# Performance work log

Hardware: AMD Instinct MI355X
Metric: run time of the kernel (lower is better)

The kernel has to match this reference:

```python
import math
import jax, jax.numpy as jnp
import numpy as np

B, N, D = 256, 64, 64
H, HEAD = D // 4, 4
UNTANH = 0.6
SHARPNESS = 1.0
BSCALE = math.sqrt(2 + math.sqrt(2))
INPUT_DIM = 100
SINK_ITERS = 10
EPS = 1e-8


def buntanh(x, a, s):
    # blended (bounded + un-)tanh: tanh(x) + a*x, variance-rescaled
    return (jnp.tanh(x) + a * x) / s


def rms_norm(x, axes):
    return x * jax.lax.rsqrt(jnp.mean(x * x, axis=axes, keepdims=True) + 1e-6)


def sinkhorn_knopp(x, iters=SINK_ITERS):
    # stable exp then alternating row/col normalization -> ~doubly stochastic
    p = jnp.exp(x - jnp.max(x, axis=(-1, -2), keepdims=True))
    def body(p, _):
        p = p / (jnp.sum(p, axis=-1, keepdims=True) + EPS)
        p = p / (jnp.sum(p, axis=-2, keepdims=True) + EPS)
        return p, None
    p, _ = jax.lax.scan(body, p, None, length=iters)
    return p


def setup_inputs() -> dict:
    key = jax.random.key(0)
    k1, k2, k3, k4, k5 = jax.random.split(key, 5)
    env_input = jax.random.normal(k1, (B, INPUT_DIM), dtype=jnp.float32)
    state = 1e-5 * jax.random.normal(k2, (B, N, D), dtype=jnp.float32)
    scale = 1.0 / math.sqrt(D)
    w1 = jax.random.normal(k3, (B, N, D, D), dtype=jnp.float32) * scale
    w2 = jax.random.normal(k4, (B, N, D, D), dtype=jnp.float32) * scale
    w3 = jax.random.normal(k5, (B, N, D, D), dtype=jnp.float32) * scale
    return {"env_input": env_input, "state": state, "w1": w1, "w2": w2, "w3": w3}


def reference(env_input, state, w1, w2, w3):
    step_state = state  # buffer clone
    prediction = buntanh(jnp.einsum('bnj,bnjk->bnk', step_state, w1), UNTANH, BSCALE)
    keys = buntanh(jnp.einsum('bnj,bnjk->bnk', step_state, w2), UNTANH, BSCALE)
    queries = buntanh(jnp.einsum('bnj,bnjk->bnk', step_state, w3), UNTANH, BSCALE)

    # torch.no_grad() block -> stop_gradient over the whole routing/target calc
    Q = queries.reshape(B, N, H, HEAD).transpose(0, 2, 1, 3)  # [B,H,N,hd]
    K = keys.reshape(B, N, H, HEAD).transpose(0, 2, 1, 3)
    V = prediction.reshape(B, N, H, HEAD).transpose(0, 2, 1, 3)
    raw_A = jnp.einsum('bhnd,bhmd->bhnm', Q, K) / math.sqrt(HEAD)
    raw_A = rms_norm(raw_A, axes=(-1, -2)) * SHARPNESS
    probs = sinkhorn_knopp(raw_A)
    A = jnp.where(probs > 1.0 / N, probs, 0.0)  # sinkhot forward (k-hot)
    routed_V = jnp.einsum('bhnm,bhmd->bhnd', A, V)
    target = routed_V.transpose(0, 2, 1, 3).reshape(B, N, D)

    num_input_nodes = math.ceil(INPUT_DIM / D)
    pad_len = num_input_nodes * D - INPUT_DIM
    env_pad = jnp.pad(env_input, ((0, 0), (0, pad_len))).reshape(B, num_input_nodes, D)
    target = target.at[:, :num_input_nodes, :].set(env_pad)
    target = jax.lax.stop_gradient(target)

    loss_w1 = jnp.mean((prediction - target) ** 2)
    loss_w2 = jnp.mean((keys - step_state) ** 2)
    loss_w3 = jnp.mean((queries - target) ** 2)
    return loss_w1 + loss_w2 + loss_w3
```

## Files before the change

### kernel.cpp

```cpp
#include <hip/hip_runtime.h>
#include <math.h>

#define TOT (256*64*64)
#define EPS_SINK 1e-8f
#define THR (1.0f/64.0f)
#define INV_BSCALE 0.5412658773652741f
#define UNTANH_A 0.6f

typedef float nativef4 __attribute__((ext_vector_type(4)));

static __device__ __forceinline__ float buntanh(float x) {
    return (tanhf(x) + UNTANH_A * x) * INV_BSCALE;
}

#if __has_builtin(__builtin_amdgcn_rcpf)
static __device__ __forceinline__ float fastrcp(float x) {
    return __builtin_amdgcn_rcpf(x);
}
#else
static __device__ __forceinline__ float fastrcp(float x) { return 1.0f / x; }
#endif

__global__ __launch_bounds__(512, 4) void fused_brain_kernel(
    const float* __restrict__ env, const float* __restrict__ state,
    const float* __restrict__ w1, const float* __restrict__ w2,
    const float* __restrict__ w3, float* __restrict__ part)
{
    __shared__ float Ss[64][65];
    __shared__ float Vh[64][33];
    __shared__ float Kh[64][33];
    __shared__ float Qh[64][33];
    __shared__ float redL[8][3];

    const int b    = blockIdx.x >> 1;
    const int half = blockIdx.x & 1;
    const int wave = threadIdx.x >> 6;
    const int l    = threadIdx.x & 63;
    const int r8   = l >> 3;
    const int c8   = l & 7;

    {
        const float* sb = state + (size_t)b * 4096 + threadIdx.x * 8;
        const float4 v0 = *(const float4*)(sb);
        const float4 v1 = *(const float4*)(sb + 4);
        const int row = threadIdx.x >> 3;
        const int col = (threadIdx.x & 7) * 8;
        Ss[row][col + 0] = v0.x; Ss[row][col + 1] = v0.y;
        Ss[row][col + 2] = v0.z; Ss[row][col + 3] = v0.w;
        Ss[row][col + 4] = v1.x; Ss[row][col + 5] = v1.y;
        Ss[row][col + 6] = v1.z; Ss[row][col + 7] = v1.w;
    }
    __syncthreads();

    for (int tt = 0; tt < 24; ++tt) {
        const int task = wave * 24 + tt;
        const int widx = task >> 6;
        const int n    = task & 63;
        const float* __restrict__ w =
            (widx == 0) ? w1 : (widx == 1) ? w2 : w3;
        const float* wp = w + ((size_t)(b * 64 + n)) * 4096 + half * 32 + 4 * c8;

        float a0 = 0.f, a1 = 0.f, a2 = 0.f, a3 = 0.f;
#pragma unroll
        for (int j0 = 0; j0 < 64; j0 += 8) {
            const nativef4 wv =
                __builtin_nontemporal_load((const nativef4*)(wp + (j0 + r8) * 64));
            const float sj = Ss[n][j0 + r8];
            a0 = fmaf(sj, wv.x, a0);
            a1 = fmaf(sj, wv.y, a1);
            a2 = fmaf(sj, wv.z, a2);
            a3 = fmaf(sj, wv.w, a3);
        }
        a0 += __shfl_xor(a0, 8, 64); a0 += __shfl_xor(a0, 16, 64); a0 += __shfl_xor(a0, 32, 64);
        a1 += __shfl_xor(a1, 8, 64); a1 += __shfl_xor(a1, 16, 64); a1 += __shfl_xor(a1, 32, 64);
        a2 += __shfl_xor(a2, 8, 64); a2 += __shfl_xor(a2, 16, 64); a2 += __shfl_xor(a2, 32, 64);
        a3 += __shfl_xor(a3, 8, 64); a3 += __shfl_xor(a3, 16, 64); a3 += __shfl_xor(a3, 32, 64);
        a0 = buntanh(a0); a1 = buntanh(a1); a2 = buntanh(a2); a3 = buntanh(a3);
        if (r8 == 0) {
            float* dst = (widx == 0) ? &Vh[n][4 * c8]
                       : (widx == 1) ? &Kh[n][4 * c8] : &Qh[n][4 * c8];
            dst[0] = a0; dst[1] = a1; dst[2] = a2; dst[3] = a3;
        }
    }
    __syncthreads();

    const int cb = 4 * wave;
    const int rg = r8, cg = c8;

    float p[8][8];
    float ss = 0.f, mx = -1e30f;
    {
        float kq[8][4];
#pragma unroll
        for (int j = 0; j < 8; ++j)
#pragma unroll
            for (int d = 0; d < 4; ++d)
                kq[j][d] = Kh[8 * cg + j][cb + d];
#pragma unroll
        for (int i = 0; i < 8; ++i) {
            const float q0 = Qh[8 * rg + i][cb + 0];
            const float q1 = Qh[8 * rg + i][cb + 1];
            const float q2 = Qh[8 * rg + i][cb + 2];
            const float q3 = Qh[8 * rg + i][cb + 3];
#pragma unroll
            for (int j = 0; j < 8; ++j) {
                const float e = (q0 * kq[j][0] + q1 * kq[j][1] +
                                 q2 * kq[j][2] + q3 * kq[j][3]) * 0.5f;
                p[i][j] = e;
                ss += e * e;
                mx = fmaxf(mx, e);
            }
        }
    }
#pragma unroll
    for (int o = 1; o <= 32; o <<= 1) {
        ss += __shfl_xor(ss, o, 64);
        mx = fmaxf(mx, __shfl_xor(mx, o, 64));
    }
    const float scale = rsqrtf(ss * (1.0f / 4096.0f) + 1e-6f);

#pragma unroll
    for (int i = 0; i < 8; ++i)
#pragma unroll
        for (int j = 0; j < 8; ++j)
            p[i][j] = __expf(scale * (p[i][j] - mx));

    for (int it = 0; it < 10; ++it) {
#pragma unroll
        for (int i = 0; i < 8; ++i) {
            float r = ((p[i][0] + p[i][1]) + (p[i][2] + p[i][3])) +
                      ((p[i][4] + p[i][5]) + (p[i][6] + p[i][7]));
            r += __shfl_xor(r, 1, 64);
            r += __shfl_xor(r, 2, 64);
            r += __shfl_xor(r, 4, 64);
            const float inv = fastrcp(r + EPS_SINK);
#pragma unroll
            for (int j = 0; j < 8; ++j) p[i][j] *= inv;
        }
#pragma unroll
        for (int j = 0; j < 8; ++j) {
            float c = ((p[0][j] + p[1][j]) + (p[2][j] + p[3][j])) +
                      ((p[4][j] + p[5][j]) + (p[6][j] + p[7][j]));
            c += __shfl_xor(c, 8, 64);
            c += __shfl_xor(c, 16, 64);
            c += __shfl_xor(c, 32, 64);
            const float inv = fastrcp(c + EPS_SINK);
#pragma unroll
            for (int i = 0; i < 8; ++i) p[i][j] *= inv;
        }
    }

#pragma unroll
    for (int i = 0; i < 8; ++i)
#pragma unroll
        for (int j = 0; j < 8; ++j)
            p[i][j] = (p[i][j] > THR) ? p[i][j] : 0.f;

    float o8[8][4];
#pragma unroll
    for (int i = 0; i < 8; ++i)
#pragma unroll
        for (int d = 0; d < 4; ++d) o8[i][d] = 0.f;
#pragma unroll
    for (int jh = 0; jh < 8; jh += 4) {
        float vf[4][4];
#pragma unroll
        for (int j = 0; j < 4; ++j)
#pragma unroll
            for (int d = 0; d < 4; ++d)
                vf[j][d] = Vh[8 * cg + jh + j][cb + d];
#pragma unroll
        for (int i = 0; i < 8; ++i)
#pragma unroll
            for (int j = 0; j < 4; ++j) {
                o8[i][0] = fmaf(p[i][jh + j], vf[j][0], o8[i][0]);
                o8[i][1] = fmaf(p[i][jh + j], vf[j][1], o8[i][1]);
                o8[i][2] = fmaf(p[i][jh + j], vf[j][2], o8[i][2]);
                o8[i][3] = fmaf(p[i][jh + j], vf[j][3], o8[i][3]);
            }
    }
#pragma unroll
    for (int i = 0; i < 8; ++i)
#pragma unroll
        for (int d = 0; d < 4; ++d) {
            float v = o8[i][d];
            v += __shfl_xor(v, 1, 64);
            v += __shfl_xor(v, 2, 64);
            v += __shfl_xor(v, 4, 64);
            o8[i][d] = v;
        }

    float tva0 = o8[0][0], tva1 = o8[0][1], tva2 = o8[0][2], tva3 = o8[0][3];
#pragma unroll
    for (int i = 1; i < 8; ++i) {
        if (cg == i) {
            tva0 = o8[i][0]; tva1 = o8[i][1];
            tva2 = o8[i][2]; tva3 = o8[i][3];
        }
    }

    float l1 = 0.f, l2 = 0.f, l3 = 0.f;
    {
        const int n = 8 * rg + cg;
#pragma unroll
        for (int d = 0; d < 4; ++d) {
            const int cl = cb + d;
            const int c  = half * 32 + cl;
            float tv;
            if (n < 2) {
                const int idx = n * 64 + c;
                tv = (idx < 100) ? env[b * 100 + idx] : 0.f;
            } else {
                tv = (d == 0) ? tva0 : (d == 1) ? tva1 : (d == 2) ? tva2 : tva3;
            }
            const float pv = Vh[n][cl];
            const float kk = Kh[n][cl];
            const float qv = Qh[n][cl];
            const float sv = Ss[n][c];
            const float d1 = pv - tv;
            const float d2 = kk - sv;
            const float d3 = qv - tv;
            l1 = fmaf(d1, d1, l1);
            l2 = fmaf(d2, d2, l2);
            l3 = fmaf(d3, d3, l3);
        }
    }
#pragma unroll
    for (int o = 1; o <= 32; o <<= 1) {
        l1 += __shfl_xor(l1, o, 64);
        l2 += __shfl_xor(l2, o, 64);
        l3 += __shfl_xor(l3, o, 64);
    }
    if (l == 0) { redL[wave][0] = l1; redL[wave][1] = l2; redL[wave][2] = l3; }
    __syncthreads();
    if (threadIdx.x == 0) {
        float s1 = 0.f, s2 = 0.f, s3 = 0.f;
#pragma unroll
        for (int wv = 0; wv < 8; ++wv) {
            s1 += redL[wv][0]; s2 += redL[wv][1]; s3 += redL[wv][2];
        }
        part[blockIdx.x]        = s1;
        part[512 + blockIdx.x]  = s2;
        part[1024 + blockIdx.x] = s3;
    }
}

__global__ __launch_bounds__(256) void loss_final_kernel(
    const float* __restrict__ part, float* __restrict__ out)
{
    float a = 0.f;
    for (int i = threadIdx.x; i < 1536; i += 256) a += part[i];
#pragma unroll
    for (int o = 32; o >= 1; o >>= 1) a += __shfl_xor(a, o, 64);
    __shared__ float red[4];
    const int wv = threadIdx.x >> 6, ln = threadIdx.x & 63;
    if (ln == 0) red[wv] = a;
    __syncthreads();
    if (threadIdx.x == 0) {
        out[0] = (red[0] + red[1] + red[2] + red[3]) * (1.0f / (float)TOT);
    }
}

extern "C" void kernel_launch(void* const* d_in, const int* in_sizes, int n_in,
                              void* d_out, int out_size, void* d_ws, size_t ws_size,
                              hipStream_t stream)
{
    const float* env   = (const float*)d_in[0];
    const float* state = (const float*)d_in[1];
    const float* w1    = (const float*)d_in[2];
    const float* w2    = (const float*)d_in[3];
    const float* w3    = (const float*)d_in[4];
    float* out = (float*)d_out;
    float* part = (float*)d_ws;

    hipLaunchKernelGGL(fused_brain_kernel, dim3(512), dim3(512), 0, stream,
                       env, state, w1, w2, w3, part);
    hipLaunchKernelGGL(loss_final_kernel, dim3(1), dim3(256), 0, stream,
                       part, out);
}
```

Baseline: 180.4 us.

## Process one batch per 1024-thread block, dropping the half-split and shared state tile

```diff
diff --git a/kernel.cpp b/kernel.cpp
--- a/kernel.cpp
+++ b/kernel.cpp
@@ -21,71 +21,69 @@
 static __device__ __forceinline__ float fastrcp(float x) { return 1.0f / x; }
 #endif
 
-__global__ __launch_bounds__(512, 4) void fused_brain_kernel(
+__global__ __launch_bounds__(1024, 4) void fused_brain_kernel(
     const float* __restrict__ env, const float* __restrict__ state,
     const float* __restrict__ w1, const float* __restrict__ w2,
     const float* __restrict__ w3, float* __restrict__ part)
 {
-    __shared__ float Ss[64][65];
-    __shared__ float Vh[64][33];
-    __shared__ float Kh[64][33];
-    __shared__ float Qh[64][33];
-    __shared__ float redL[8][3];
-
-    const int b    = blockIdx.x >> 1;
-    const int half = blockIdx.x & 1;
+    __shared__ float Vh[64][65];
+    __shared__ float Kh[64][65];
+    __shared__ float Qh[64][65];
+    __shared__ float redL[16][3];
+
+    const int b    = blockIdx.x;
     const int wave = threadIdx.x >> 6;
     const int l    = threadIdx.x & 63;
-    const int r8   = l >> 3;
-    const int c8   = l & 7;
-
-    {
-        const float* sb = state + (size_t)b * 4096 + threadIdx.x * 8;
-        const float4 v0 = *(const float4*)(sb);
-        const float4 v1 = *(const float4*)(sb + 4);
-        const int row = threadIdx.x >> 3;
-        const int col = (threadIdx.x & 7) * 8;
-        Ss[row][col + 0] = v0.x; Ss[row][col + 1] = v0.y;
-        Ss[row][col + 2] = v0.z; Ss[row][col + 3] = v0.w;
-        Ss[row][col + 4] = v1.x; Ss[row][col + 5] = v1.y;
-        Ss[row][col + 6] = v1.z; Ss[row][col + 7] = v1.w;
-    }
-    __syncthreads();
-
-    for (int tt = 0; tt < 24; ++tt) {
-        const int task = wave * 24 + tt;
+    const int k4   = l & 15;
+    const int jg   = l >> 4;
+
+#pragma unroll 2
+    for (int tt = 0; tt < 12; ++tt) {
+        const int task = wave * 12 + tt;
         const int widx = task >> 6;
         const int n    = task & 63;
         const float* __restrict__ w =
             (widx == 0) ? w1 : (widx == 1) ? w2 : w3;
-        const float* wp = w + ((size_t)(b * 64 + n)) * 4096 + half * 32 + 4 * c8;
-
+        const size_t bn = (size_t)(b * 64 + n);
+
+        const float* sp = state + bn * 64 + jg * 16;
+        float s[16];
+#pragma unroll
+        for (int i = 0; i < 4; ++i) {
+            const float4 v = *(const float4*)(sp + 4 * i);
+            s[4 * i + 0] = v.x; s[4 * i + 1] = v.y;
+            s[4 * i + 2] = v.z; s[4 * i + 3] = v.w;
+        }
+
+        const nativef4* wp = (const nativef4*)(w + bn * 4096 +
+                                               (size_t)(jg * 16) * 64 + k4 * 4);
         float a0 = 0.f, a1 = 0.f, a2 = 0.f, a3 = 0.f;
 #pragma unroll
-        for (int j0 = 0; j0 < 64; j0 += 8) {
-            const nativef4 wv =
-                __builtin_nontemporal_load((const nativef4*)(wp + (j0 + r8) * 64));
-            const float sj = Ss[n][j0 + r8];
-            a0 = fmaf(sj, wv.x, a0);
-            a1 = fmaf(sj, wv.y, a1);
-            a2 = fmaf(sj, wv.z, a2);
-            a3 = fmaf(sj, wv.w, a3);
-        }
-        a0 += __shfl_xor(a0, 8, 64); a0 += __shfl_xor(a0, 16, 64); a0 += __shfl_xor(a0, 32, 64);
-        a1 += __shfl_xor(a1, 8, 64); a1 += __shfl_xor(a1, 16, 64); a1 += __shfl_xor(a1, 32, 64);
-        a2 += __shfl_xor(a2, 8, 64); a2 += __shfl_xor(a2, 16, 64); a2 += __shfl_xor(a2, 32, 64);
-        a3 += __shfl_xor(a3, 8, 64); a3 += __shfl_xor(a3, 16, 64); a3 += __shfl_xor(a3, 32, 64);
-        a0 = buntanh(a0); a1 = buntanh(a1); a2 = buntanh(a2); a3 = buntanh(a3);
-        if (r8 == 0) {
-            float* dst = (widx == 0) ? &Vh[n][4 * c8]
-                       : (widx == 1) ? &Kh[n][4 * c8] : &Qh[n][4 * c8];
-            dst[0] = a0; dst[1] = a1; dst[2] = a2; dst[3] = a3;
+        for (int jj = 0; jj < 16; ++jj) {
+            const nativef4 wv = __builtin_nontemporal_load(wp + jj * 16);
+            a0 = fmaf(s[jj], wv.x, a0);
+            a1 = fmaf(s[jj], wv.y, a1);
+            a2 = fmaf(s[jj], wv.z, a2);
+            a3 = fmaf(s[jj], wv.w, a3);
+        }
+        a0 += __shfl_xor(a0, 16, 64); a0 += __shfl_xor(a0, 32, 64);
+        a1 += __shfl_xor(a1, 16, 64); a1 += __shfl_xor(a1, 32, 64);
+        a2 += __shfl_xor(a2, 16, 64); a2 += __shfl_xor(a2, 32, 64);
+        a3 += __shfl_xor(a3, 16, 64); a3 += __shfl_xor(a3, 32, 64);
+        if (jg == 0) {
+            float* dst = (widx == 0) ? &Vh[n][4 * k4]
+                       : (widx == 1) ? &Kh[n][4 * k4] : &Qh[n][4 * k4];
+            dst[0] = buntanh(a0);
+            dst[1] = buntanh(a1);
+            dst[2] = buntanh(a2);
+            dst[3] = buntanh(a3);
         }
     }
     __syncthreads();
 
     const int cb = 4 * wave;
-    const int rg = r8, cg = c8;
+    const int rg = l >> 3;
+    const int cg = l & 7;
 
     float p[8][8];
     float ss = 0.f, mx = -1e30f;
@@ -202,10 +200,10 @@
     float l1 = 0.f, l2 = 0.f, l3 = 0.f;
     {
         const int n = 8 * rg + cg;
+        const float* srow = state + ((size_t)(b * 64 + n)) * 64;
 #pragma unroll
         for (int d = 0; d < 4; ++d) {
-            const int cl = cb + d;
-            const int c  = half * 32 + cl;
+            const int c = cb + d;
             float tv;
             if (n < 2) {
                 const int idx = n * 64 + c;
@@ -213,10 +211,10 @@
             } else {
                 tv = (d == 0) ? tva0 : (d == 1) ? tva1 : (d == 2) ? tva2 : tva3;
             }
-            const float pv = Vh[n][cl];
-            const float kk = Kh[n][cl];
-            const float qv = Qh[n][cl];
-            const float sv = Ss[n][c];
+            const float pv = Vh[n][c];
+            const float kk = Kh[n][c];
+            const float qv = Qh[n][c];
+            const float sv = srow[c];
             const float d1 = pv - tv;
             const float d2 = kk - sv;
             const float d3 = qv - tv;
@@ -236,12 +234,12 @@
     if (threadIdx.x == 0) {
         float s1 = 0.f, s2 = 0.f, s3 = 0.f;
 #pragma unroll
-        for (int wv = 0; wv < 8; ++wv) {
+        for (int wv = 0; wv < 16; ++wv) {
             s1 += redL[wv][0]; s2 += redL[wv][1]; s3 += redL[wv][2];
         }
-        part[blockIdx.x]        = s1;
-        part[512 + blockIdx.x]  = s2;
-        part[1024 + blockIdx.x] = s3;
+        part[b]       = s1;
+        part[256 + b] = s2;
+        part[512 + b] = s3;
     }
 }
 
@@ -249,7 +247,7 @@
     const float* __restrict__ part, float* __restrict__ out)
 {
     float a = 0.f;
-    for (int i = threadIdx.x; i < 1536; i += 256) a += part[i];
+    for (int i = threadIdx.x; i < 768; i += 256) a += part[i];
 #pragma unroll
     for (int o = 32; o >= 1; o >>= 1) a += __shfl_xor(a, o, 64);
     __shared__ float red[4];
@@ -273,7 +271,7 @@
     float* out = (float*)d_out;
     float* part = (float*)d_ws;
 
-    hipLaunchKernelGGL(fused_brain_kernel, dim3(512), dim3(512), 0, stream,
+    hipLaunchKernelGGL(fused_brain_kernel, dim3(256), dim3(1024), 0, stream,
                        env, state, w1, w2, w3, part);
     hipLaunchKernelGGL(loss_final_kernel, dim3(1), dim3(256), 0, stream,
                        part, out);
```

Result: faster. 168.1 us (-6.8%).
